# Optimization experiments

Hardware: AMD Instinct MI355X
Metric: run time of the kernel (lower is better)

Reference implementation:

```python
import jax, jax.numpy as jnp
import numpy as np

SEQ, BATCH, EMBED = 2048, 4, 768
NUM_HEADS = 12
HEAD_DIM = EMBED // NUM_HEADS
SCALING = HEAD_DIM ** -0.5


def setup_inputs() -> dict:
    key = jax.random.key(0)
    ks = jax.random.split(key, 9)
    std = 0.02
    d = {"x": jax.random.normal(ks[0], (SEQ, BATCH, EMBED), dtype=jnp.float32)}
    for i, n in enumerate(["q", "k", "v", "out"]):
        d[f"W{n}"] = jax.random.normal(ks[1 + 2 * i], (EMBED, EMBED), dtype=jnp.float32) * std
        d[f"b{n}"] = jax.random.normal(ks[2 + 2 * i], (EMBED,), dtype=jnp.float32) * std
    return d


def reference(x, Wq, bq, Wk, bk, Wv, bv, Wout, bout):
    # x: [tgt_len, bsz, embed_dim] (fairseq seq-first layout per forward body)
    T, B, E = x.shape
    H, Dh = NUM_HEADS, HEAD_DIM

    q = (x @ Wq.T + bq) * SCALING          # [T, B, E]
    k = x @ Wk.T + bk
    v = x @ Wv.T + bv

    # view(T, B*H, Dh).transpose(0, 1) -> [B*H, T, Dh]
    q = q.reshape(T, B * H, Dh).transpose(1, 0, 2)
    k = k.reshape(T, B * H, Dh).transpose(1, 0, 2)
    v = v.reshape(T, B * H, Dh).transpose(1, 0, 2)

    # bmm: [B*H, T, T] attention scores (full O(T^2) matrix, as in the original)
    scores = jnp.einsum('bqd,bkd->bqk', q, k)
    # util_softmax with onnx_trace=True: softmax in float32, then cast back
    probs = jax.nn.softmax(scores.astype(jnp.float32), axis=-1).astype(scores.dtype)
    # dropout p=0.0 -> identity

    attn = jnp.einsum('bqk,bkd->bqd', probs, v)           # [B*H, T, Dh]
    attn = attn.transpose(1, 0, 2).reshape(T, B, E)       # [T, B, E]
    return attn @ Wout.T + bout
```

## Files before the change

### kernel.cpp

```cpp
#include <hip/hip_runtime.h>
#include <hip/hip_bf16.h>

#define SEQ 2048
#define BATCH 4
#define EMBED 768
#define NHEAD 12
#define HDIM 64
#define NROWS (SEQ*BATCH)
#define GH (BATCH*NHEAD)
#define KVBLK 64

typedef __bf16 bf16;
typedef __attribute__((ext_vector_type(4))) __bf16 bf16x4;
typedef __attribute__((ext_vector_type(8))) __bf16 bf16x8;
typedef __attribute__((ext_vector_type(4))) float f32x4;
typedef __attribute__((ext_vector_type(16))) float f32x16;
typedef __attribute__((ext_vector_type(2))) unsigned uint2v;
typedef __attribute__((ext_vector_type(4))) unsigned uint4v;

#define LOG2E 1.44269504088896340736f

__global__ __launch_bounds__(256) void cvt_kernel(const float* __restrict__ in,
                                                  bf16* __restrict__ out, int n4) {
  int i = blockIdx.x * 256 + threadIdx.x;
  if (i >= n4) return;
  float4 v = reinterpret_cast<const float4*>(in)[i];
  bf16x4 o;
  o[0] = (bf16)v.x; o[1] = (bf16)v.y; o[2] = (bf16)v.z; o[3] = (bf16)v.w;
  reinterpret_cast<bf16x4*>(out)[i] = o;
}

__global__ __launch_bounds__(256) void cvt_w4(const float* __restrict__ Wq,
                                              const float* __restrict__ Wk,
                                              const float* __restrict__ Wv,
                                              const float* __restrict__ Wo,
                                              bf16* __restrict__ Wqkvb,
                                              bf16* __restrict__ Wob) {
  const int n4 = EMBED * EMBED / 4;
  int i = blockIdx.x * 256 + threadIdx.x;
  if (i >= n4) return;
  const float* src;
  bf16* dst;
  switch (blockIdx.y) {
    case 0: src = Wq; dst = Wqkvb; break;
    case 1: src = Wk; dst = Wqkvb + EMBED * EMBED; break;
    case 2: src = Wv; dst = Wqkvb + 2 * EMBED * EMBED; break;
    default: src = Wo; dst = Wob; break;
  }
  float4 v = reinterpret_cast<const float4*>(src)[i];
  bf16x4 o;
  o[0] = (bf16)v.x; o[1] = (bf16)v.y; o[2] = (bf16)v.z; o[3] = (bf16)v.w;
  reinterpret_cast<bf16x4*>(dst)[i] = o;
}

__global__ __launch_bounds__(256) void gemm_qkv(const bf16* __restrict__ A,
                                                const bf16* __restrict__ B,
                                                const float* __restrict__ bq,
                                                const float* __restrict__ bk,
                                                const float* __restrict__ bv,
                                                bf16* __restrict__ Qh,
                                                bf16* __restrict__ Kh,
                                                bf16* __restrict__ Vt) {
  constexpr int K = EMBED;
  __shared__ bf16 As[128 * 32];
  __shared__ bf16 Bs[128 * 32];
  const int tid = threadIdx.x;
  const int l = tid & 63;
  const int w = tid >> 6;
  const int row0 = blockIdx.x * 128;
  const int col0 = blockIdx.y * 128;
  const int wm = (w >> 1) * 64;
  const int wn = (w & 1) * 64;
  const int l15 = l & 15, l4 = l >> 4;

  f32x4 acc[4][4] = {};

  for (int k0 = 0; k0 < K; k0 += 32) {
#pragma unroll
    for (int i = 0; i < 2; ++i) {
      int c = tid + i * 256;
      int r = c >> 2, cc = c & 3;
      __builtin_amdgcn_global_load_lds(
          (const __attribute__((address_space(1))) void*)(A + (size_t)(row0 + r) * K + k0 + cc * 8),
          (__attribute__((address_space(3))) void*)(As + c * 8), 16, 0, 0);
    }
#pragma unroll
    for (int i = 0; i < 2; ++i) {
      int c = tid + i * 256;
      int r = c >> 2, cc = c & 3;
      __builtin_amdgcn_global_load_lds(
          (const __attribute__((address_space(1))) void*)(B + (size_t)(col0 + r) * K + k0 + cc * 8),
          (__attribute__((address_space(3))) void*)(Bs + c * 8), 16, 0, 0);
    }
    __syncthreads();

    bf16x8 af[4], bfr[4];
#pragma unroll
    for (int i = 0; i < 4; ++i)
      af[i] = *reinterpret_cast<const bf16x8*>(&As[(wm + i * 16 + l15) * 32 + l4 * 8]);
#pragma unroll
    for (int j = 0; j < 4; ++j)
      bfr[j] = *reinterpret_cast<const bf16x8*>(&Bs[(wn + j * 16 + l15) * 32 + l4 * 8]);
#pragma unroll
    for (int i = 0; i < 4; ++i)
#pragma unroll
      for (int j = 0; j < 4; ++j)
        acc[i][j] = __builtin_amdgcn_mfma_f32_16x16x32_bf16(af[i], bfr[j], acc[i][j], 0, 0, 0);
    __syncthreads();
  }

  const int sel = blockIdx.y / 6;
  const float* bias = sel == 0 ? bq : (sel == 1 ? bk : bv);
  const int colbase = col0 - sel * EMBED;
#pragma unroll
  for (int i = 0; i < 4; ++i) {
#pragma unroll
    for (int j = 0; j < 4; ++j) {
      int col = colbase + wn + j * 16 + l15;
      float bia = bias[col];
#pragma unroll
      for (int r = 0; r < 4; ++r) {
        int row = row0 + wm + i * 16 + l4 * 4 + r;
        float v = acc[i][j][r] + bia;
        int t = row >> 2, bb = row & 3;
        int hh = col >> 6, d = col & 63;
        int g = bb * NHEAD + hh;
        if (sel == 0)      Qh[((size_t)g * SEQ + t) * HDIM + d] = (bf16)(v * (0.125f * LOG2E));
        else if (sel == 1) Kh[((size_t)g * SEQ + t) * HDIM + d] = (bf16)v;
        else               Vt[((size_t)g * HDIM + d) * SEQ + t] = (bf16)v;
      }
    }
  }
}

__global__ __launch_bounds__(256) void gemm_out(const bf16* __restrict__ A,
                                                const bf16* __restrict__ B,
                                                const float* __restrict__ bias,
                                                float* __restrict__ outp) {
  constexpr int K = EMBED;
  __shared__ bf16 As[128 * 32];
  __shared__ bf16 Bs[128 * 32];
  const int tid = threadIdx.x;
  const int l = tid & 63;
  const int w = tid >> 6;
  const int row0 = blockIdx.x * 128;
  const int col0 = blockIdx.y * 128;
  const int wm = (w >> 1) * 64;
  const int wn = (w & 1) * 64;
  const int l15 = l & 15, l4 = l >> 4;

  f32x4 acc[4][4] = {};

  for (int k0 = 0; k0 < K; k0 += 32) {
#pragma unroll
    for (int i = 0; i < 2; ++i) {
      int c = tid + i * 256;
      int r = c >> 2, cc = c & 3;
      __builtin_amdgcn_global_load_lds(
          (const __attribute__((address_space(1))) void*)(A + (size_t)(row0 + r) * K + k0 + cc * 8),
          (__attribute__((address_space(3))) void*)(As + c * 8), 16, 0, 0);
    }
#pragma unroll
    for (int i = 0; i < 2; ++i) {
      int c = tid + i * 256;
      int r = c >> 2, cc = c & 3;
      __builtin_amdgcn_global_load_lds(
          (const __attribute__((address_space(1))) void*)(B + (size_t)(col0 + r) * K + k0 + cc * 8),
          (__attribute__((address_space(3))) void*)(Bs + c * 8), 16, 0, 0);
    }
    __syncthreads();

    bf16x8 af[4], bfr[4];
#pragma unroll
    for (int i = 0; i < 4; ++i)
      af[i] = *reinterpret_cast<const bf16x8*>(&As[(wm + i * 16 + l15) * 32 + l4 * 8]);
#pragma unroll
    for (int j = 0; j < 4; ++j)
      bfr[j] = *reinterpret_cast<const bf16x8*>(&Bs[(wn + j * 16 + l15) * 32 + l4 * 8]);
#pragma unroll
    for (int i = 0; i < 4; ++i)
#pragma unroll
      for (int j = 0; j < 4; ++j)
        acc[i][j] = __builtin_amdgcn_mfma_f32_16x16x32_bf16(af[i], bfr[j], acc[i][j], 0, 0, 0);
    __syncthreads();
  }

#pragma unroll
  for (int i = 0; i < 4; ++i) {
#pragma unroll
    for (int j = 0; j < 4; ++j) {
      int col = col0 + wn + j * 16 + l15;
      float bia = bias[col];
#pragma unroll
      for (int r = 0; r < 4; ++r) {
        int row = row0 + wm + i * 16 + l4 * 4 + r;
        outp[(size_t)row * EMBED + col] = acc[i][j][r] + bia;
      }
    }
  }
}

#define SWZ(r) ((((r) & 7) ^ (((r) >> 3) & 3)))
__global__ __launch_bounds__(256, 4) void attn_kernel(const bf16* __restrict__ Qh,
                                                      const bf16* __restrict__ Kh,
                                                      const bf16* __restrict__ Vt,
                                                      bf16* __restrict__ attnb) {
  const int g = blockIdx.x % GH;
  const int q0 = (blockIdx.x / GH) * 128;
  const int tid = threadIdx.x;
  const int w = tid >> 6, l = tid & 63;
  const int l31 = l & 31, l5 = l >> 5;
  const int qw = q0 + w * 32;
  const int rsw = SWZ(l31);

  __shared__ bf16 Ks[2][KVBLK * HDIM];
  __shared__ bf16 Vs[2][HDIM * KVBLK];

  const bf16* Qp = Qh + (size_t)g * SEQ * HDIM;
  const bf16* Kp = Kh + (size_t)g * SEQ * HDIM;
  const bf16* Vp = Vt + (size_t)g * HDIM * SEQ;

#define STAGE_K(buf, kv0)                                                               \
  do {                                                                                  \
    _Pragma("unroll") for (int i = 0; i < 2; ++i) {                                     \
      int t = i * 256 + tid;                                                            \
      int r_ = t >> 3, c_ = t & 7;                                                      \
      __builtin_amdgcn_global_load_lds(                                                 \
          (const __attribute__((address_space(1))) void*)(Kp + (size_t)((kv0) + r_) * HDIM + ((c_ ^ SWZ(r_)) * 8)), \
          (__attribute__((address_space(3))) void*)(&Ks[buf][t * 8]), 16, 0, 0);        \
    }                                                                                   \
  } while (0)

#define STAGE_V(buf, kv0)                                                               \
  do {                                                                                  \
    _Pragma("unroll") for (int i = 0; i < 2; ++i) {                                     \
      int t = i * 256 + tid;                                                            \
      int r_ = t >> 3, c_ = t & 7;                                                      \
      __builtin_amdgcn_global_load_lds(                                                 \
          (const __attribute__((address_space(1))) void*)(Vp + (size_t)r_ * SEQ + (kv0) + ((c_ ^ SWZ(r_)) * 8)), \
          (__attribute__((address_space(3))) void*)(&Vs[buf][t * 8]), 16, 0, 0);        \
    }                                                                                   \
  } while (0)

  bf16x8 bq[4];
#pragma unroll
  for (int m = 0; m < 4; ++m)
    bq[m] = *reinterpret_cast<const bf16x8*>(
        Qp + (size_t)(qw + l31) * HDIM + m * 16 + l5 * 8);

  bf16x8 vone;
#pragma unroll
  for (int i = 0; i < 8; ++i) vone[i] = (bf16)1.0f;

  f32x16 acco[2] = {};
  f32x16 accs = {};

  STAGE_K(0, 0);
  STAGE_V(0, 0);
  __syncthreads();

  int cur = 0;
  for (int kv0 = 0; kv0 < SEQ; kv0 += KVBLK) {
    int nxt = (kv0 + KVBLK) & (SEQ - 1);
    STAGE_V(cur ^ 1, nxt);
    STAGE_K(cur ^ 1, nxt);

#pragma unroll
    for (int h = 0; h < 2; ++h) {
      f32x16 s = {};
#pragma unroll
      for (int m = 0; m < 4; ++m) {
        bf16x8 ak = *reinterpret_cast<const bf16x8*>(
            &Ks[cur][(32 * h + l31) * 64 + (((2 * m + l5) ^ rsw) * 8)]);
        __builtin_amdgcn_s_setprio(1);
        s = __builtin_amdgcn_mfma_f32_32x32x16_bf16(ak, bq[m], s, 0, 0, 0);
        __builtin_amdgcn_s_setprio(0);
      }

      unsigned pg[8];
#pragma unroll
      for (int gq = 0; gq < 4; ++gq) {
        float p0 = exp2f(s[4 * gq + 0]);
        float p1 = exp2f(s[4 * gq + 1]);
        float p2 = exp2f(s[4 * gq + 2]);
        float p3 = exp2f(s[4 * gq + 3]);
        bf16x4 q4;
        q4[0] = (bf16)p0; q4[1] = (bf16)p1; q4[2] = (bf16)p2; q4[3] = (bf16)p3;
        uint2v d2 = __builtin_bit_cast(uint2v, q4);
        pg[2 * gq] = d2[0];
        pg[2 * gq + 1] = d2[1];
      }

#pragma unroll
      for (int j = 0; j < 2; ++j) {
        unsigned sx = l5 ? pg[4 * j + 0] : pg[4 * j + 2];
        unsigned sy = l5 ? pg[4 * j + 1] : pg[4 * j + 3];
        unsigned rx = (unsigned)__shfl_xor((int)sx, 32);
        unsigned ry = (unsigned)__shfl_xor((int)sy, 32);
        unsigned ox = l5 ? pg[4 * j + 2] : pg[4 * j + 0];
        unsigned oy = l5 ? pg[4 * j + 3] : pg[4 * j + 1];
        uint4v f;
        f[0] = l5 ? rx : ox;  f[1] = l5 ? ry : oy;
        f[2] = l5 ? ox : rx;  f[3] = l5 ? oy : ry;
        bf16x8 pb = __builtin_bit_cast(bf16x8, f);
#pragma unroll
        for (int dt = 0; dt < 2; ++dt) {
          bf16x8 av = *reinterpret_cast<const bf16x8*>(
              &Vs[cur][(dt * 32 + l31) * 64 + (((4 * h + 2 * j + l5) ^ rsw) * 8)]);
          __builtin_amdgcn_s_setprio(1);
          acco[dt] = __builtin_amdgcn_mfma_f32_32x32x16_bf16(av, pb, acco[dt], 0, 0, 0);
          __builtin_amdgcn_s_setprio(0);
        }
        __builtin_amdgcn_s_setprio(1);
        accs = __builtin_amdgcn_mfma_f32_32x32x16_bf16(vone, pb, accs, 0, 0, 0);
        __builtin_amdgcn_s_setprio(0);
      }
    }
    __syncthreads();
    cur ^= 1;
  }

  const float rinv = __builtin_amdgcn_rcpf(accs[0]);
  const int tq = qw + l31;
  const int bb = g / NHEAD, hh = g % NHEAD;
  const size_t rowbase = ((size_t)tq * BATCH + bb) * EMBED + hh * HDIM;
#pragma unroll
  for (int dt = 0; dt < 2; ++dt)
#pragma unroll
    for (int gq = 0; gq < 4; ++gq) {
      int d = dt * 32 + 8 * gq + 4 * l5;
      bf16x4 o4;
      o4[0] = (bf16)(acco[dt][4 * gq + 0] * rinv);
      o4[1] = (bf16)(acco[dt][4 * gq + 1] * rinv);
      o4[2] = (bf16)(acco[dt][4 * gq + 2] * rinv);
      o4[3] = (bf16)(acco[dt][4 * gq + 3] * rinv);
      *reinterpret_cast<bf16x4*>(attnb + rowbase + d) = o4;
    }
}

extern "C" void kernel_launch(void* const* d_in, const int* in_sizes, int n_in,
                              void* d_out, int out_size, void* d_ws, size_t ws_size,
                              hipStream_t stream) {
  const float* x  = (const float*)d_in[0];
  const float* Wq = (const float*)d_in[1];
  const float* bq = (const float*)d_in[2];
  const float* Wk = (const float*)d_in[3];
  const float* bk = (const float*)d_in[4];
  const float* Wv = (const float*)d_in[5];
  const float* bv = (const float*)d_in[6];
  const float* Wo = (const float*)d_in[7];
  const float* bo = (const float*)d_in[8];
  float* out = (float*)d_out;

  char* ws = (char*)d_ws;
  bf16* xb    = (bf16*)(ws + 0);
  bf16* Wqkvb = (bf16*)(ws + 12582912);
  bf16* Wob   = (bf16*)(ws + 16121856);
  bf16* Qh    = (bf16*)(ws + 17301504);
  bf16* Kh    = (bf16*)(ws + 29884416);
  bf16* Vt    = (bf16*)(ws + 42467328);
  bf16* attnb = (bf16*)(ws + 55050240);

  cvt_kernel<<<6144, 256, 0, stream>>>(x, xb, NROWS * EMBED / 4);
  cvt_w4<<<dim3(576, 4), 256, 0, stream>>>(Wq, Wk, Wv, Wo, Wqkvb, Wob);

  gemm_qkv<<<dim3(NROWS / 128, 18), 256, 0, stream>>>(xb, Wqkvb, bq, bk, bv, Qh, Kh, Vt);

  attn_kernel<<<GH * (SEQ / 128), 256, 0, stream>>>(Qh, Kh, Vt, attnb);

  gemm_out<<<dim3(NROWS / 128, EMBED / 128), 256, 0, stream>>>(attnb, Wob, bo, out);
}
```

Baseline: 175.2 us.

## Triple-buffer K/V staging with one barrier and split MFMA accumulator chains

```diff
diff --git a/kernel.cpp b/kernel.cpp
--- a/kernel.cpp
+++ b/kernel.cpp
@@ -19,6 +19,7 @@
 typedef __attribute__((ext_vector_type(4))) unsigned uint4v;
 
 #define LOG2E 1.44269504088896340736f
+#define SWZ(r) ((((r) & 7) ^ (((r) >> 3) & 3)))
 
 __global__ __launch_bounds__(256) void cvt_kernel(const float* __restrict__ in,
                                                   bf16* __restrict__ out, int n4) {
@@ -200,7 +201,6 @@
   }
 }
 
-#define SWZ(r) ((((r) & 7) ^ (((r) >> 3) & 3)))
 __global__ __launch_bounds__(256, 4) void attn_kernel(const bf16* __restrict__ Qh,
                                                       const bf16* __restrict__ Kh,
                                                       const bf16* __restrict__ Vt,
@@ -213,8 +213,8 @@
   const int qw = q0 + w * 32;
   const int rsw = SWZ(l31);
 
-  __shared__ bf16 Ks[2][KVBLK * HDIM];
-  __shared__ bf16 Vs[2][HDIM * KVBLK];
+  __shared__ bf16 Ks[3][KVBLK * HDIM];
+  __shared__ bf16 Vs[3][HDIM * KVBLK];
 
   const bf16* Qp = Qh + (size_t)g * SEQ * HDIM;
   const bf16* Kp = Kh + (size_t)g * SEQ * HDIM;
@@ -252,38 +252,48 @@
 #pragma unroll
   for (int i = 0; i < 8; ++i) vone[i] = (bf16)1.0f;
 
-  f32x16 acco[2] = {};
-  f32x16 accs = {};
+  f32x16 accoJ[2][2] = {};
+  f32x16 accsJ[2] = {};
 
   STAGE_K(0, 0);
   STAGE_V(0, 0);
-  __syncthreads();
 
   int cur = 0;
-  for (int kv0 = 0; kv0 < SEQ; kv0 += KVBLK) {
-    int nxt = (kv0 + KVBLK) & (SEQ - 1);
-    STAGE_V(cur ^ 1, nxt);
-    STAGE_K(cur ^ 1, nxt);
+  for (int t = 0; t < SEQ / KVBLK; ++t) {
+    const int nxt = (cur == 2) ? 0 : cur + 1;
+    const int nkv = ((t + 1) & (SEQ / KVBLK - 1)) * KVBLK;
+    STAGE_K(nxt, nkv);
+    STAGE_V(nxt, nkv);
+    asm volatile("s_waitcnt vmcnt(4)" ::: "memory");
+    __builtin_amdgcn_s_barrier();
 
 #pragma unroll
     for (int h = 0; h < 2; ++h) {
-      f32x16 s = {};
-#pragma unroll
-      for (int m = 0; m < 4; ++m) {
+      f32x16 s_lo = {}, s_hi = {};
+#pragma unroll
+      for (int m = 0; m < 2; ++m) {
         bf16x8 ak = *reinterpret_cast<const bf16x8*>(
             &Ks[cur][(32 * h + l31) * 64 + (((2 * m + l5) ^ rsw) * 8)]);
         __builtin_amdgcn_s_setprio(1);
-        s = __builtin_amdgcn_mfma_f32_32x32x16_bf16(ak, bq[m], s, 0, 0, 0);
+        s_lo = __builtin_amdgcn_mfma_f32_32x32x16_bf16(ak, bq[m], s_lo, 0, 0, 0);
         __builtin_amdgcn_s_setprio(0);
       }
+#pragma unroll
+      for (int m = 2; m < 4; ++m) {
+        bf16x8 ak = *reinterpret_cast<const bf16x8*>(
+            &Ks[cur][(32 * h + l31) * 64 + (((2 * m + l5) ^ rsw) * 8)]);
+        __builtin_amdgcn_s_setprio(1);
+        s_hi = __builtin_amdgcn_mfma_f32_32x32x16_bf16(ak, bq[m], s_hi, 0, 0, 0);
+        __builtin_amdgcn_s_setprio(0);
+      }
 
       unsigned pg[8];
 #pragma unroll
       for (int gq = 0; gq < 4; ++gq) {
-        float p0 = exp2f(s[4 * gq + 0]);
-        float p1 = exp2f(s[4 * gq + 1]);
-        float p2 = exp2f(s[4 * gq + 2]);
-        float p3 = exp2f(s[4 * gq + 3]);
+        float p0 = exp2f(s_lo[4 * gq + 0] + s_hi[4 * gq + 0]);
+        float p1 = exp2f(s_lo[4 * gq + 1] + s_hi[4 * gq + 1]);
+        float p2 = exp2f(s_lo[4 * gq + 2] + s_hi[4 * gq + 2]);
+        float p3 = exp2f(s_lo[4 * gq + 3] + s_hi[4 * gq + 3]);
         bf16x4 q4;
         q4[0] = (bf16)p0; q4[1] = (bf16)p1; q4[2] = (bf16)p2; q4[3] = (bf16)p3;
         uint2v d2 = __builtin_bit_cast(uint2v, q4);
@@ -308,19 +318,18 @@
           bf16x8 av = *reinterpret_cast<const bf16x8*>(
               &Vs[cur][(dt * 32 + l31) * 64 + (((4 * h + 2 * j + l5) ^ rsw) * 8)]);
           __builtin_amdgcn_s_setprio(1);
-          acco[dt] = __builtin_amdgcn_mfma_f32_32x32x16_bf16(av, pb, acco[dt], 0, 0, 0);
+          accoJ[j][dt] = __builtin_amdgcn_mfma_f32_32x32x16_bf16(av, pb, accoJ[j][dt], 0, 0, 0);
           __builtin_amdgcn_s_setprio(0);
         }
         __builtin_amdgcn_s_setprio(1);
-        accs = __builtin_amdgcn_mfma_f32_32x32x16_bf16(vone, pb, accs, 0, 0, 0);
+        accsJ[j] = __builtin_amdgcn_mfma_f32_32x32x16_bf16(vone, pb, accsJ[j], 0, 0, 0);
         __builtin_amdgcn_s_setprio(0);
       }
     }
-    __syncthreads();
-    cur ^= 1;
-  }
-
-  const float rinv = __builtin_amdgcn_rcpf(accs[0]);
+    cur = nxt;
+  }
+
+  const float rinv = __builtin_amdgcn_rcpf(accsJ[0][0] + accsJ[1][0]);
   const int tq = qw + l31;
   const int bb = g / NHEAD, hh = g % NHEAD;
   const size_t rowbase = ((size_t)tq * BATCH + bb) * EMBED + hh * HDIM;
@@ -330,10 +339,10 @@
     for (int gq = 0; gq < 4; ++gq) {
       int d = dt * 32 + 8 * gq + 4 * l5;
       bf16x4 o4;
-      o4[0] = (bf16)(acco[dt][4 * gq + 0] * rinv);
-      o4[1] = (bf16)(acco[dt][4 * gq + 1] * rinv);
-      o4[2] = (bf16)(acco[dt][4 * gq + 2] * rinv);
-      o4[3] = (bf16)(acco[dt][4 * gq + 3] * rinv);
+      o4[0] = (bf16)((accoJ[0][dt][4 * gq + 0] + accoJ[1][dt][4 * gq + 0]) * rinv);
+      o4[1] = (bf16)((accoJ[0][dt][4 * gq + 1] + accoJ[1][dt][4 * gq + 1]) * rinv);
+      o4[2] = (bf16)((accoJ[0][dt][4 * gq + 2] + accoJ[1][dt][4 * gq + 2]) * rinv);
+      o4[3] = (bf16)((accoJ[0][dt][4 * gq + 3] + accoJ[1][dt][4 * gq + 3]) * rinv);
       *reinterpret_cast<bf16x4*>(attnb + rowbase + d) = o4;
     }
 }
```

Result: slower. 209.4 us (+19.5%).
